# Performance work log

Measured on AMD Instinct MI355X. Metric: run time of the kernel, lower is better.

Reference implementation:

```python
import jax, jax.numpy as jnp
import numpy as np

BS, Hq, Wq = 4, 64, 64
C, M, K, L = 256, 8, 4, 4
CV = C // M
SCALES = [(64, 64), (32, 32), (16, 16), (8, 8)]


def grid_sample_nhwc(img, grid):
    """torch.F.grid_sample(mode='bilinear', padding_mode='zeros', align_corners=False).
    img: [N,h,w,Cf], grid: [N,H,W,2] with (x,y) in [-1,1]. Returns [N,H,W,Cf]."""
    N, h, w, _ = img.shape
    x = (grid[..., 0] + 1.0) * (w * 0.5) - 0.5
    y = (grid[..., 1] + 1.0) * (h * 0.5) - 0.5
    x0 = jnp.floor(x)
    y0 = jnp.floor(y)
    wx1 = x - x0
    wy1 = y - y0
    wx0 = 1.0 - wx1
    wy0 = 1.0 - wy1
    b = jnp.arange(N)[:, None, None]

    def gather(yi, xi):
        valid = ((xi >= 0) & (xi < w) & (yi >= 0) & (yi < h)).astype(img.dtype)
        xi_c = jnp.clip(xi, 0, w - 1).astype(jnp.int32)
        yi_c = jnp.clip(yi, 0, h - 1).astype(jnp.int32)
        return img[b, yi_c, xi_c] * valid[..., None]  # [N,H,W,Cf]

    return (gather(y0, x0) * (wy0 * wx0)[..., None]
            + gather(y0, x0 + 1.0) * (wy0 * wx1)[..., None]
            + gather(y0 + 1.0, x0) * (wy1 * wx0)[..., None]
            + gather(y0 + 1.0, x0 + 1.0) * (wy1 * wx1)[..., None])


def _forward(q, feats, ref, Wz, bz, Wo, bo, Wa, ba, Wp, bp, Wm, bm):
    BM = BS * M
    z = q @ Wz + bz  # [BS,H,W,C]
    # learned offsets: [BS,H,W,2MKL] -> [BS,M,L,K,H,W,2] -> [BM,L,K,H,W,2]
    off = (z @ Wo + bo).reshape(BS, Hq, Wq, M, L, K, 2)
    off = off.transpose(0, 3, 4, 5, 1, 2, 6).reshape(BM, L, K, Hq, Wq, 2)
    # attention weights over the L*K samples per head
    attn = jax.nn.softmax((z @ Wa + ba).reshape(BS, Hq, Wq, M, L * K), axis=-1)
    attn = attn.transpose(0, 3, 1, 2, 4).reshape(BM, Hq * Wq, L * K)

    samples = []
    for l, f in enumerate(feats):
        h, w = f.shape[1], f.shape[2]
        # value projection, split heads: [BS,h,w,C] -> [BM,h,w,CV] (BS outer, M inner)
        wp = (f @ Wp + bp).reshape(BS, h, w, M, CV).transpose(0, 3, 1, 2, 4).reshape(BM, h, w, CV)
        # phi(h,w,ref) then .repeat(M,1,1,1): tile with M as the OUTER axis (faithful to source)
        pref = jnp.stack([ref[..., 0] * (w - 1), ref[..., 1] * (h - 1)], axis=-1)  # [BS,H,W,2]
        pref = jnp.tile(pref, (M, 1, 1, 1))  # [BM,H,W,2]
        pts = pref[:, None] + off[:, l]  # [BM,K,H,W,2]
        gx = 2.0 * pts[..., 0] / max(w - 1, 1) - 1.0
        gy = 2.0 * pts[..., 1] / max(h - 1, 1) - 1.0
        grid = jnp.stack([gx, gy], axis=-1)  # [BM,K,H,W,2]
        s = jax.vmap(grid_sample_nhwc, in_axes=(None, 1), out_axes=0)(wp, grid)  # [K,BM,H,W,CV]
        samples.append(s.transpose(1, 4, 2, 0, 3))  # [BM,CV,H,K,W] == torch.stack(..., dim=3)

    sf = jnp.stack(samples, axis=1)  # [BM,L,CV,H,K,W]
    # faithful to source: permute(0,4,5,3,1,2) then raw view to [BM, H*W, CV, L*K]
    sf = sf.transpose(0, 4, 5, 3, 1, 2).reshape(BM, Hq * Wq, CV, L * K)
    out = jnp.einsum('nlds,nls->nld', sf, attn)  # [BM,HW,CV]
    out = out.reshape(BS, M, Hq, Wq, CV).transpose(0, 2, 3, 1, 4).reshape(BS, Hq, Wq, C)
    return out @ Wm + bm


def setup_inputs() -> dict:
    key = jax.random.key(0)
    ks = jax.random.split(key, 12)
    s = 0.02
    inp = {
        'q': jax.random.normal(ks[0], (BS, Hq, Wq, C), jnp.float32),
        'ref': jax.random.uniform(ks[1], (BS, Hq, Wq, 2), jnp.float32),
    }
    for i, (h, w) in enumerate(SCALES):
        inp[f'feat{i}'] = jax.random.normal(jax.random.fold_in(ks[2], i), (BS, h, w, C), jnp.float32)
    inp['Wz'] = jax.random.normal(ks[3], (C, C), jnp.float32) * s
    inp['bz'] = jnp.zeros((C,), jnp.float32)
    inp['Wo'] = jax.random.normal(ks[4], (C, 2 * M * K * L), jnp.float32) * s
    inp['bo'] = jnp.zeros((2 * M * K * L,), jnp.float32)
    inp['Wa'] = jax.random.normal(ks[5], (C, M * K * L), jnp.float32) * s
    inp['ba'] = jnp.zeros((M * K * L,), jnp.float32)
    inp['Wp'] = jax.random.normal(ks[6], (C, C), jnp.float32) * s
    inp['bp'] = jnp.zeros((C,), jnp.float32)
    inp['Wm'] = jax.random.normal(ks[7], (C, C), jnp.float32) * s
    inp['bm'] = jnp.zeros((C,), jnp.float32)
    return inp


def reference(q, feat0, feat1, feat2, feat3, ref, Wz, bz, Wo, bo, Wa, ba, Wp, bp, Wm, bm):
    return _forward(q, [feat0, feat1, feat2, feat3], ref, Wz, bz, Wo, bo, Wa, ba, Wp, bp, Wm, bm)
```

## Files before the change

### kernel.cpp

```cpp
#include <hip/hip_runtime.h>
#include <hip/hip_bf16.h>


typedef __attribute__((ext_vector_type(8))) _Float16 half8;
typedef __attribute__((ext_vector_type(2))) _Float16 half2t;
typedef __attribute__((ext_vector_type(4))) float f32x4;

#if __has_builtin(__builtin_amdgcn_fdot2)
__device__ __forceinline__ float fdot2f(half2t a, half2t b, float c) {
    return __builtin_amdgcn_fdot2(a, b, c, false);
}
#else
__device__ __forceinline__ float fdot2f(half2t a, half2t b, float c) {
    return c + (float)a.x * (float)b.x + (float)a.y * (float)b.y;
}
#endif

#define GLOAD_LDS16(gp, lp)                                                      \
    __builtin_amdgcn_global_load_lds(                                            \
        (const __attribute__((address_space(1))) void*)(gp),                     \
        (__attribute__((address_space(3))) void*)(lp), 16, 0, 0)

__device__ __forceinline__ int swz(int row, int sem_q) {
    return row * 32 + ((sem_q ^ (row & 3)) * 8);
}

__global__ __launch_bounds__(256) void transpose_w(
    const float* __restrict__ Wz, const float* __restrict__ Wo,
    const float* __restrict__ Wa, const float* __restrict__ Wp,
    const float* __restrict__ Wm,
    _Float16* __restrict__ Wzt, _Float16* __restrict__ Woat,
    _Float16* __restrict__ Wpt, _Float16* __restrict__ Wmt)
{
    __shared__ float ts[64][65];
    const int bid = blockIdx.x;
    const float* src; _Float16* dst; int N, tile;
    if      (bid < 16) { src = Wz; dst = Wzt;          N = 256; tile = bid; }
    else if (bid < 32) { src = Wo; dst = Woat;         N = 256; tile = bid - 16; }
    else if (bid < 40) { src = Wa; dst = Woat + 65536; N = 128; tile = bid - 32; }
    else if (bid < 56) { src = Wp; dst = Wpt;          N = 256; tile = bid - 40; }
    else               { src = Wm; dst = Wmt;          N = 256; tile = bid - 56; }
    const int ntn = N >> 6;
    const int k0 = (tile / ntn) * 64, n0 = (tile % ntn) * 64;
    const int t = threadIdx.x, tx = t & 63, ty = t >> 6;
    #pragma unroll
    for (int r = 0; r < 16; ++r) {
        const int kk = r * 4 + ty;
        ts[kk][tx] = src[(size_t)(k0 + kk) * N + n0 + tx];
    }
    __syncthreads();
    #pragma unroll
    for (int r = 0; r < 16; ++r) {
        const int nn = r * 4 + ty;
        dst[(size_t)(n0 + nn) * 256 + k0 + tx] = (_Float16)ts[tx][nn];
    }
}

template<typename AT>
__device__ __forceinline__ void gemm_core(
    _Float16* __restrict__ As, _Float16* __restrict__ Bs,
    const AT* __restrict__ A, const _Float16* __restrict__ Bt,
    int m0, int n0, f32x4 (&acc)[4][4])
{
    const int t    = threadIdx.x;
    const int lane = t & 63, wid = t >> 6;
    const int wr = wid >> 1, wc = wid & 1;
    const int lr = lane & 15, sq = lane >> 4;

    const int grow = lane >> 2;
    const int gqs  = (lane & 3) ^ ((lane >> 2) & 3);

    for (int kt = 0; kt < 256; kt += 32) {
        if constexpr (sizeof(AT) == 4) {
            const int arow = t >> 1, ac = t & 1;
            const float* ap = (const float*)A + (size_t)(m0 + arow) * 256 + kt + ac * 16;
            float v[16];
            #pragma unroll
            for (int i = 0; i < 4; ++i) {
                float4 f = ((const float4*)ap)[i];
                v[4*i] = f.x; v[4*i+1] = f.y; v[4*i+2] = f.z; v[4*i+3] = f.w;
            }
            half8 h0, h1;
            #pragma unroll
            for (int i = 0; i < 8; ++i) { h0[i] = (_Float16)v[i]; h1[i] = (_Float16)v[8+i]; }
            *(half8*)&As[swz(arow, ac * 2)]     = h0;
            *(half8*)&As[swz(arow, ac * 2 + 1)] = h1;
        } else {
            #pragma unroll
            for (int h = 0; h < 2; ++h) {
                const int rbase = wid * 32 + h * 16;
                const _Float16* ga = (const _Float16*)A +
                    (size_t)(m0 + rbase + grow) * 256 + kt + gqs * 8;
                GLOAD_LDS16(ga, &As[rbase * 32]);
            }
        }
        #pragma unroll
        for (int h = 0; h < 2; ++h) {
            const int rbase = wid * 32 + h * 16;
            const _Float16* gb = Bt +
                (size_t)(n0 + rbase + grow) * 256 + kt + gqs * 8;
            GLOAD_LDS16(gb, &Bs[rbase * 32]);
        }
        __syncthreads();

        half8 af[4], bf[4];
        #pragma unroll
        for (int m = 0; m < 4; ++m)
            af[m] = *(const half8*)&As[swz(wr*64 + m*16 + lr, sq)];
        #pragma unroll
        for (int n = 0; n < 4; ++n)
            bf[n] = *(const half8*)&Bs[swz(wc*64 + n*16 + lr, sq)];
        #pragma unroll
        for (int m = 0; m < 4; ++m)
            #pragma unroll
            for (int n = 0; n < 4; ++n)
                acc[m][n] = __builtin_amdgcn_mfma_f32_16x16x32_f16(af[m], bf[n], acc[m][n], 0, 0, 0);
        __syncthreads();
    }
}

__device__ __forceinline__ void epi_f16(
    f32x4 (&acc)[4][4], const float* __restrict__ bias,
    _Float16* __restrict__ C, int N, int m0, int n0)
{
    const int t = threadIdx.x, lane = t & 63, wid = t >> 6;
    const int wr = wid >> 1, wc = wid & 1, lr = lane & 15;
    #pragma unroll
    for (int n = 0; n < 4; ++n) {
        const int col = n0 + wc*64 + n*16 + lr;
        const float bv = bias[col];
        #pragma unroll
        for (int m = 0; m < 4; ++m)
            #pragma unroll
            for (int r = 0; r < 4; ++r) {
                const int row = m0 + wr*64 + m*16 + (lane >> 4)*4 + r;
                C[(size_t)row * N + col] = (_Float16)(acc[m][n][r] + bv);
            }
    }
}

__device__ __forceinline__ void epi_wp(
    f32x4 (&acc)[4][4], const float* __restrict__ bias,
    _Float16* __restrict__ C, int m0, int n0, int shift)
{
    const int t = threadIdx.x, lane = t & 63, wid = t >> 6;
    const int wr = wid >> 1, wc = wid & 1, lr = lane & 15;
    const int mask = (1 << shift) - 1;
    #pragma unroll
    for (int n = 0; n < 4; ++n) {
        const int col = n0 + wc*64 + n*16 + lr;
        const float bv = bias[col];
        const int mh = col >> 5, cv = col & 31;
        #pragma unroll
        for (int m = 0; m < 4; ++m)
            #pragma unroll
            for (int r = 0; r < 4; ++r) {
                const int row = m0 + wr*64 + m*16 + (lane >> 4)*4 + r;
                const int bb = row >> shift, pix = row & mask;
                C[((((size_t)(bb * 8 + mh)) << shift) + pix) * 32 + cv] =
                    (_Float16)(acc[m][n][r] + bv);
            }
    }
}

__global__ __launch_bounds__(256) void gemm_z_wp(
    const float* __restrict__ q, const _Float16* __restrict__ Wzt,
    const float* __restrict__ bz, _Float16* __restrict__ z,
    const float* __restrict__ f0, const float* __restrict__ f1,
    const float* __restrict__ f2, const float* __restrict__ f3,
    const _Float16* __restrict__ Wpt, const float* __restrict__ bp,
    _Float16* __restrict__ w0, _Float16* __restrict__ w1,
    _Float16* __restrict__ w2, _Float16* __restrict__ w3)
{
    __shared__ _Float16 As[128 * 32];
    __shared__ _Float16 Bs[128 * 32];
    const int by = blockIdx.y, bx = blockIdx.x;
    f32x4 acc[4][4] = {};
    if (by < 128) {
        gemm_core<float>(As, Bs, q, Wzt, by * 128, bx * 128, acc);
        epi_f16(acc, bz, z, 256, by * 128, bx * 128);
    } else {
        const int y = by - 128;
        const float* A; _Float16* C; int m0, shift;
        if      (y < 128) { A = f0; C = w0; m0 = y * 128;         shift = 12; }
        else if (y < 160) { A = f1; C = w1; m0 = (y - 128) * 128; shift = 10; }
        else if (y < 168) { A = f2; C = w2; m0 = (y - 160) * 128; shift = 8;  }
        else              { A = f3; C = w3; m0 = (y - 168) * 128; shift = 6;  }
        gemm_core<float>(As, Bs, A, Wpt, m0, bx * 128, acc);
        epi_wp(acc, bp, C, m0, bx * 128, shift);
    }
}

__global__ __launch_bounds__(256) void gemm_zo_at(
    const _Float16* __restrict__ z, const _Float16* __restrict__ Woat,
    const float* __restrict__ bo, const float* __restrict__ ba,
    _Float16* __restrict__ zo, _Float16* __restrict__ attn)
{
    __shared__ __align__(16) char ldsbuf[128 * 136 * 2];
    _Float16* As = (_Float16*)ldsbuf;
    _Float16* Bs = As + 128 * 32;
    _Float16 (*smax)[136] = (_Float16(*)[136])ldsbuf;

    const int bx = blockIdx.x, by = blockIdx.y;
    const int m0 = by * 128;
    f32x4 acc[4][4] = {};
    gemm_core<_Float16>(As, Bs, z, Woat, m0, bx * 128, acc);

    const int t = threadIdx.x, lane = t & 63, wid = t >> 6;
    const int wr = wid >> 1, wc = wid & 1, lr = lane & 15;

    if (bx < 2) {
        #pragma unroll
        for (int n = 0; n < 4; ++n) {
            const int c = bx * 128 + wc*64 + n*16 + lr;
            const float bv = bo[c];
            const int cp = (((c >> 3) & 3) << 6) | ((c >> 5) << 3)
                         | (((c >> 1) & 3) << 1) | (c & 1);
            #pragma unroll
            for (int m = 0; m < 4; ++m)
                #pragma unroll
                for (int r = 0; r < 4; ++r) {
                    const int row = m0 + wr*64 + m*16 + (lane >> 4)*4 + r;
                    zo[(size_t)row * 256 + cp] = (_Float16)(acc[m][n][r] + bv);
                }
        }
    } else {
        __syncthreads();
        #pragma unroll
        for (int n = 0; n < 4; ++n) {
            const int col = wc*64 + n*16 + lr;
            const float bv = ba[col];
            #pragma unroll
            for (int m = 0; m < 4; ++m)
                #pragma unroll
                for (int r = 0; r < 4; ++r) {
                    const int rowl = wr*64 + m*16 + (lane >> 4)*4 + r;
                    smax[rowl][col] = (_Float16)(acc[m][n][r] + bv);
                }
        }
        __syncthreads();
        #pragma unroll
        for (int j = 0; j < 4; ++j) {
            const int g    = j * 256 + t;
            const int rowl = g >> 3, mh = g & 7;
            const half8* sp = (const half8*)&smax[rowl][mh * 16];
            const half8 a = sp[0], bb8 = sp[1];
            float v[16];
            #pragma unroll
            for (int i = 0; i < 8; ++i) { v[i] = (float)a[i]; v[8+i] = (float)bb8[i]; }
            float mx = v[0];
            #pragma unroll
            for (int i = 1; i < 16; ++i) mx = fmaxf(mx, v[i]);
            float s = 0.f;
            #pragma unroll
            for (int i = 0; i < 16; ++i) { v[i] = expf(v[i] - mx); s += v[i]; }
            const float inv = 1.f / s;
            half8 o0, o1;
            #pragma unroll
            for (int i = 0; i < 8; ++i) { o0[i] = (_Float16)(v[i]*inv); o1[i] = (_Float16)(v[8+i]*inv); }
            const int row  = m0 + rowl;
            const int qpos = row & 4095, b = row >> 12;
            const int k = qpos >> 10, qx = (qpos >> 4) & 63, ya = qpos & 15;
            half8* op = (half8*)(attn +
                ((((((size_t)b * 64 + qx) * 16 + ya) * 8 + mh) * 4 + k) * 16));
            op[0] = o0; op[1] = o1;
        }
    }
}

__global__ __launch_bounds__(256) void sample9(
    const _Float16* __restrict__ zo,
    const _Float16* __restrict__ attn,
    const float* __restrict__ ref,
    const _Float16* __restrict__ wp0, const _Float16* __restrict__ wp1,
    const _Float16* __restrict__ wp2, const _Float16* __restrict__ wp3,
    _Float16* __restrict__ outp)
{
    const int bid = blockIdx.x;
    const int bp_ = (bid & 7) * 1024 + (bid >> 3);
    const int t  = threadIdx.x;
    const int k  = t & 3;
    const int m  = (t >> 2) & 7;
    const int qp = (t >> 5) & 1;
    const int l  = t >> 6;

    const int query = bp_ * 2 + qp;
    const int qx = query & 63;
    const int qy = (query >> 6) & 63;
    const int b  = query >> 12;

    const int ya = qy >> 2, yb = qy & 3;
    const int p  = (k << 10) | (qx << 4) | ya;
    const int cb = m * 32 + yb * 8 + l * 2;

    const int hw = 64 >> l;
    const int shift = 12 - 2 * l;
    const float fw = (float)hw;
    const _Float16* wp = (l == 0) ? wp0 : (l == 1) ? wp1 : (l == 2) ? wp2 : wp3;

    const unsigned off2 = *(const unsigned*)(zo + (size_t)query * 256 + (l * 64 + m * 8 + k * 2));
    const half2t offh = __builtin_bit_cast(half2t, off2);
    const float offx = (float)offh.x;
    const float offy = (float)offh.y;

    const int rb = m & 3;
    const float2 rr = *(const float2*)(ref + ((size_t)(rb * 4096) + qy * 64 + qx) * 2);

    const float px  = rr.x * (fw - 1.f) + offx;
    const float py  = rr.y * (fw - 1.f) + offy;
    const float gx  = 2.f * px / (fw - 1.f) - 1.f;
    const float gy  = 2.f * py / (fw - 1.f) - 1.f;
    const float xim = (gx + 1.f) * (fw * 0.5f) - 0.5f;
    const float yim = (gy + 1.f) * (fw * 0.5f) - 0.5f;

    const float x0f = floorf(xim), y0f = floorf(yim);
    const float wx1 = xim - x0f, wy1 = yim - y0f;
    const float wx0 = 1.f - wx1, wy0 = 1.f - wy1;
    const int ix0 = (int)x0f, iy0 = (int)y0f;

    half2t w[8];
    {
        const uint4* ap = (const uint4*)(attn +
            ((((((size_t)b * 64 + qx) * 16 + ya) * 8 + m) * 4 + k) * 16));
        const uint4 wa = ap[0], wb = ap[1];
        w[0] = __builtin_bit_cast(half2t, wa.x); w[1] = __builtin_bit_cast(half2t, wa.y);
        w[2] = __builtin_bit_cast(half2t, wa.z); w[3] = __builtin_bit_cast(half2t, wa.w);
        w[4] = __builtin_bit_cast(half2t, wb.x); w[5] = __builtin_bit_cast(half2t, wb.y);
        w[6] = __builtin_bit_cast(half2t, wb.z); w[7] = __builtin_bit_cast(half2t, wb.w);
    }

    const _Float16* plane = wp + ((((size_t)(b * 8 + m)) << shift) * 32);

    float wtv[4];
    uint4 u[4][4];
    #pragma unroll
    for (int tap = 0; tap < 4; ++tap) {
        int iy = iy0 + (tap >> 1);
        int ix = ix0 + (tap & 1);
        const bool ok = (iy >= 0) & (iy < hw) & (ix >= 0) & (ix < hw);
        float wt = ((tap >> 1) ? wy1 : wy0) * ((tap & 1) ? wx1 : wx0);
        wtv[tap] = ok ? wt : 0.f;
        iy = min(max(iy, 0), hw - 1);
        ix = min(max(ix, 0), hw - 1);
        const uint4* tp = (const uint4*)(plane + ((size_t)(iy * hw + ix)) * 32);
        u[tap][0] = tp[0]; u[tap][1] = tp[1]; u[tap][2] = tp[2]; u[tap][3] = tp[3];
    }

    float r0 = 0.f, r1 = 0.f;
    #pragma unroll
    for (int tap = 0; tap < 4; ++tap) {
        float d0 = 0.f, d1 = 0.f;
        d0 = fdot2f(__builtin_bit_cast(half2t, u[tap][0].x), w[0], d0);
        d0 = fdot2f(__builtin_bit_cast(half2t, u[tap][0].y), w[1], d0);
        d0 = fdot2f(__builtin_bit_cast(half2t, u[tap][0].z), w[2], d0);
        d0 = fdot2f(__builtin_bit_cast(half2t, u[tap][0].w), w[3], d0);
        d0 = fdot2f(__builtin_bit_cast(half2t, u[tap][1].x), w[4], d0);
        d0 = fdot2f(__builtin_bit_cast(half2t, u[tap][1].y), w[5], d0);
        d0 = fdot2f(__builtin_bit_cast(half2t, u[tap][1].z), w[6], d0);
        d0 = fdot2f(__builtin_bit_cast(half2t, u[tap][1].w), w[7], d0);
        d1 = fdot2f(__builtin_bit_cast(half2t, u[tap][2].x), w[0], d1);
        d1 = fdot2f(__builtin_bit_cast(half2t, u[tap][2].y), w[1], d1);
        d1 = fdot2f(__builtin_bit_cast(half2t, u[tap][2].z), w[2], d1);
        d1 = fdot2f(__builtin_bit_cast(half2t, u[tap][2].w), w[3], d1);
        d1 = fdot2f(__builtin_bit_cast(half2t, u[tap][3].x), w[4], d1);
        d1 = fdot2f(__builtin_bit_cast(half2t, u[tap][3].y), w[5], d1);
        d1 = fdot2f(__builtin_bit_cast(half2t, u[tap][3].z), w[6], d1);
        d1 = fdot2f(__builtin_bit_cast(half2t, u[tap][3].w), w[7], d1);
        r0 += wtv[tap] * d0;
        r1 += wtv[tap] * d1;
    }

    half2t o; o.x = (_Float16)r0; o.y = (_Float16)r1;
    *(half2t*)(outp + ((size_t)b * 4096 + p) * 256 + cb) = o;
}

__global__ __launch_bounds__(256) void gemm_final(
    const _Float16* __restrict__ A, const _Float16* __restrict__ Wmt,
    const float* __restrict__ bias, float* __restrict__ C)
{
    __shared__ _Float16 As[128 * 32];
    __shared__ _Float16 Bs[128 * 32];
    const int m0 = blockIdx.y * 128, n0 = blockIdx.x * 128;
    f32x4 acc[4][4] = {};
    gemm_core<_Float16>(As, Bs, A, Wmt, m0, n0, acc);
    const int t = threadIdx.x, lane = t & 63, wid = t >> 6;
    const int wr = wid >> 1, wc = wid & 1, lr = lane & 15;
    #pragma unroll
    for (int n = 0; n < 4; ++n) {
        const int col = n0 + wc*64 + n*16 + lr;
        const float bv = bias[col];
        #pragma unroll
        for (int m = 0; m < 4; ++m)
            #pragma unroll
            for (int r = 0; r < 4; ++r) {
                const int row = m0 + wr*64 + m*16 + (lane >> 4)*4 + r;
                C[(size_t)row * 256 + col] = acc[m][n][r] + bv;
            }
    }
}

extern "C" void kernel_launch(void* const* d_in, const int* in_sizes, int n_in,
                              void* d_out, int out_size, void* d_ws, size_t ws_size,
                              hipStream_t stream)
{
    const float* q   = (const float*)d_in[0];
    const float* ref = (const float*)d_in[1];
    const float* f0  = (const float*)d_in[2];
    const float* f1  = (const float*)d_in[3];
    const float* f2  = (const float*)d_in[4];
    const float* f3  = (const float*)d_in[5];
    const float* Wz  = (const float*)d_in[6];
    const float* bz  = (const float*)d_in[7];
    const float* Wo  = (const float*)d_in[8];
    const float* bo  = (const float*)d_in[9];
    const float* Wa  = (const float*)d_in[10];
    const float* ba  = (const float*)d_in[11];
    const float* Wp  = (const float*)d_in[12];
    const float* bp  = (const float*)d_in[13];
    const float* Wm  = (const float*)d_in[14];
    const float* bm  = (const float*)d_in[15];
    float* out = (float*)d_out;

    char* ws = (char*)d_ws;
    _Float16* z    = (_Float16*)(ws + ((size_t)0));
    _Float16* zo   = (_Float16*)(ws + ((size_t)16 << 20));
    _Float16* attn = (_Float16*)(ws + ((size_t)24 << 20));
    _Float16* wp0  = (_Float16*)(ws + ((size_t)28 << 20));
    _Float16* wp1  = (_Float16*)(ws + ((size_t)36 << 20));
    _Float16* wp2  = (_Float16*)(ws + ((size_t)38 << 20));
    _Float16* wp3  = (_Float16*)(ws + ((size_t)38 << 20) + ((size_t)512 << 10));
    _Float16* Wzt  = (_Float16*)(ws + ((size_t)40 << 20));
    _Float16* Woat = (_Float16*)(ws + ((size_t)40 << 20) + ((size_t)256 << 10));
    _Float16* Wpt  = (_Float16*)(ws + ((size_t)40 << 20) + ((size_t)768 << 10));
    _Float16* Wmt  = (_Float16*)(ws + ((size_t)41 << 20));
    _Float16* outp = z;

    const dim3 blk(256);

    transpose_w<<<dim3(72), blk, 0, stream>>>(Wz, Wo, Wa, Wp, Wm, Wzt, Woat, Wpt, Wmt);
    gemm_z_wp<<<dim3(2, 298), blk, 0, stream>>>(q, Wzt, bz, z,
                                                f0, f1, f2, f3, Wpt, bp,
                                                wp0, wp1, wp2, wp3);
    gemm_zo_at<<<dim3(3, 128), blk, 0, stream>>>(z, Woat, bo, ba, zo, attn);
    sample9<<<dim3(8192), blk, 0, stream>>>(zo, attn, ref, wp0, wp1, wp2, wp3, outp);
    gemm_final<<<dim3(2, 128), blk, 0, stream>>>(outp, Wmt, bm, out);
}
```

Measured before the change: 89.07 us.

## Stage sampler outputs in LDS to write full contiguous output rows

The sampling kernel now uses 512-thread blocks covering four query rows (all yb) so that each block produces four complete 256-channel output rows. Results go into a padded shared-memory buffer and, after a barrier, are written back as fully coalesced 512-byte rows instead of scattered 4-byte stores. This trades one __syncthreads and larger blocks, which may lower occupancy, for better global write coalescing.

```diff
diff --git a/kernel.cpp b/kernel.cpp
--- a/kernel.cpp
+++ b/kernel.cpp
@@ -268,7 +268,7 @@
     }
 }
 
-__global__ __launch_bounds__(256) void sample9(
+__global__ __launch_bounds__(512) void sample10(
     const _Float16* __restrict__ zo,
     const _Float16* __restrict__ attn,
     const float* __restrict__ ref,
@@ -276,22 +276,23 @@
     const _Float16* __restrict__ wp2, const _Float16* __restrict__ wp3,
     _Float16* __restrict__ outp)
 {
+    __shared__ unsigned srow[4 * 129];
+
     const int bid = blockIdx.x;
-    const int bp_ = (bid & 7) * 1024 + (bid >> 3);
+    const int blk = (bid & 7) * 512 + (bid >> 3);
+    const int qx = (blk >> 4) & 63;
+    const int ya = blk & 15;
+    const int b  = blk >> 10;
+
     const int t  = threadIdx.x;
     const int k  = t & 3;
     const int m  = (t >> 2) & 7;
-    const int qp = (t >> 5) & 1;
-    const int l  = t >> 6;
-
-    const int query = bp_ * 2 + qp;
-    const int qx = query & 63;
-    const int qy = (query >> 6) & 63;
-    const int b  = query >> 12;
-
-    const int ya = qy >> 2, yb = qy & 3;
+    const int yb = (t >> 5) & 3;
+    const int l  = t >> 7;
+
+    const int qy = ya * 4 + yb;
+    const int query = b * 4096 + qy * 64 + qx;
     const int p  = (k << 10) | (qx << 4) | ya;
-    const int cb = m * 32 + yb * 8 + l * 2;
 
     const int hw = 64 >> l;
     const int shift = 12 - 2 * l;
@@ -370,8 +371,16 @@
         r1 += wtv[tap] * d1;
     }
 
-    half2t o; o.x = (_Float16)r0; o.y = (_Float16)r1;
-    *(half2t*)(outp + ((size_t)b * 4096 + p) * 256 + cb) = o;
+    half2t pr; pr.x = (_Float16)r0; pr.y = (_Float16)r1;
+    srow[k * 129 + (m * 16 + yb * 4 + l)] = __builtin_bit_cast(unsigned, pr);
+    __syncthreads();
+
+    {
+        const int ro = t >> 7;
+        const int e  = t & 127;
+        const int prow = (ro << 10) | (qx << 4) | ya;
+        ((unsigned*)(outp + ((size_t)b * 4096 + prow) * 256))[e] = srow[ro * 129 + e];
+    }
 }
 
 __global__ __launch_bounds__(256) void gemm_final(
@@ -442,6 +451,6 @@
                                                 f0, f1, f2, f3, Wpt, bp,
                                                 wp0, wp1, wp2, wp3);
     gemm_zo_at<<<dim3(3, 128), blk, 0, stream>>>(z, Woat, bo, ba, zo, attn);
-    sample9<<<dim3(8192), blk, 0, stream>>>(zo, attn, ref, wp0, wp1, wp2, wp3, outp);
+    sample10<<<dim3(4096), dim3(512), 0, stream>>>(zo, attn, ref, wp0, wp1, wp2, wp3, outp);
     gemm_final<<<dim3(2, 128), blk, 0, stream>>>(outp, Wmt, bm, out);
 }
```

Measured after the change: 84.44 us. 5.2% less time.
